# Kernel tuning notes

Hardware: AMD Instinct MI355X
Metric: run time of the kernel (lower is better)

The kernel has to match this reference:

```python
import jax, jax.numpy as jnp
import numpy as np

S, B, E = 2048, 8, 1024  # seq_len, batch, embed_dim
GAMMA = 0.5              # Kernel(gamma=0.5)


def setup_inputs() -> dict:
    key = jax.random.key(0)
    ks = jax.random.split(key, 4)
    # Weight scale 1/E keeps pairwise squared distances O(1) so the RBF
    # kernel weights are well-conditioned (exp doesn't underflow to all-zeros).
    w_scale = 1.0 / E
    inputs = jax.random.normal(ks[0], (S, B, E), dtype=jnp.float32)
    Wq = jax.random.normal(ks[1], (E, E), dtype=jnp.float32) * w_scale
    Wk = jax.random.normal(ks[2], (E, E), dtype=jnp.float32) * w_scale
    Wv = jax.random.normal(ks[3], (E, E), dtype=jnp.float32) * w_scale
    bq = jnp.zeros((E,), jnp.float32)
    bk = jnp.zeros((E,), jnp.float32)
    bv = jnp.zeros((E,), jnp.float32)
    return {"inputs": inputs, "Wq": Wq, "bq": bq, "Wk": Wk, "bk": bk,
            "Wv": Wv, "bv": bv}


def reference(inputs, Wq, bq, Wk, bk, Wv, bv):
    # QKV projections (nn.Linear: x @ W.T + b)
    q = inputs @ Wq.T + bq  # (S, B, E)
    k = inputs @ Wk.T + bk  # (S, B, E)
    v = inputs @ Wv.T + bv  # (S, B, E)

    # Pairwise RBF kernel sim[t, j, b] = exp(-gamma * ||q[t,b] - k[j,b]||^2)
    # (vectorized replacement of the original O(S^2) python double loop),
    # via ||q||^2 + ||k||^2 - 2 q.k expansion (GEMM-shaped contraction).
    q2 = jnp.sum(q * q, axis=-1)                 # (S, B)
    k2 = jnp.sum(k * k, axis=-1)                 # (S, B)
    qk = jnp.einsum('tbe,jbe->tjb', q, k)        # (S, S, B)
    d2 = q2[:, None, :] + k2[None, :, :] - 2.0 * qk
    d2 = jnp.maximum(d2, 0.0)

    # sim / sim.sum(dim=1) with sim = exp(-gamma*d2) is exactly
    # softmax(-gamma*d2) over axis 1 (the j axis) -- numerically stable form.
    sim = jax.nn.softmax(-GAMMA * d2, axis=1)    # (S, S, B): (t, j, b)

    # Aggregate values: out[t, b, e] = sum_j sim[t, j, b] * v[j, b, e]
    return jnp.einsum('tjb,jbe->tbe', sim, v)    # (S, B, E)
```

## Files before the change

### kernel.cpp

```cpp
#include <hip/hip_runtime.h>
#include <stdint.h>

#define S_LEN 2048
#define BATCH 8
#define EMB   1024
#define GAMMA 0.5f

typedef unsigned short ushort_t;
typedef __attribute__((ext_vector_type(8))) short  short8;
typedef __attribute__((ext_vector_type(8))) unsigned short ushort8;
typedef __attribute__((ext_vector_type(4))) float  floatx4;

__device__ __forceinline__ ushort_t f2bf(float f) {
  uint32_t x = __float_as_uint(f);
  x += 0x7fffu + ((x >> 16) & 1u);
  return (ushort_t)(x >> 16);
}

__device__ __forceinline__ void gl_lds16(const ushort_t* g, ushort_t* l) {
  __builtin_amdgcn_global_load_lds(
      (const __attribute__((address_space(1))) unsigned int*)g,
      (__attribute__((address_space(3))) unsigned int*)l, 16, 0, 0);
}


__device__ __forceinline__ void stage_half(const ushort_t* __restrict__ G,
                                           int ld, int kcol,
                                           ushort_t* lregion, int wave, int lane) {
  const int r4 = lane >> 2;
  const int slot = (lane & 3) ^ ((r4 >> 1) & 3);
  const ushort_t* g = G + (size_t)(wave * 32 + r4) * ld + kcol + slot * 8;
  gl_lds16(g, lregion + wave * 1024);
  gl_lds16(g + (size_t)16 * ld, lregion + wave * 1024 + 512);
}

__device__ __forceinline__ short8 lds_frag(const ushort_t* region, int row, int q) {
  return *(const short8*)(region + row * 32 + (((q ^ (row >> 1)) & 3) << 3));
}

#define MFMA_PH(J0, J1)                                                        \
  __builtin_amdgcn_s_barrier();                                                \
  asm volatile("s_waitcnt lgkmcnt(0)" ::: "memory");                           \
  __builtin_amdgcn_sched_barrier(0);                                           \
  __builtin_amdgcn_s_setprio(1);                                               \
  _Pragma("unroll")                                                            \
  for (int i = 0; i < 8; ++i) {                                                \
    acc[i][J0] = __builtin_amdgcn_mfma_f32_16x16x32_bf16(ar[i], b0, acc[i][J0], 0, 0, 0); \
    acc[i][J1] = __builtin_amdgcn_mfma_f32_16x16x32_bf16(ar[i], b1, acc[i][J1], 0, 0, 0); \
  }                                                                            \
  __builtin_amdgcn_s_setprio(0);

__device__ __forceinline__ void gemm8_core(
    const ushort_t* __restrict__ A, const ushort_t* __restrict__ B,
    int lda, int ldb, int K, ushort_t* smem, floatx4 (&acc)[8][4])
{
  const int tid = threadIdx.x;
  const int wave = tid >> 6, lane = tid & 63;
  const int wm = wave >> 2, wn = wave & 3;
  const int lr = lane & 15, q = lane >> 4;
  const int NT = K >> 6;

  stage_half(A, lda, 0,  smem +     0, wave, lane);
  stage_half(B, ldb, 0,  smem + 16384, wave, lane);
  stage_half(A, lda, 32, smem +  8192, wave, lane);
  stage_half(B, ldb, 32, smem + 24576, wave, lane);
  stage_half(A, lda, 64, smem + 32768, wave, lane);
  stage_half(B, ldb, 64, smem + 49152, wave, lane);
  stage_half(A, lda, 96, smem + 40960, wave, lane);
  asm volatile("s_waitcnt vmcnt(6)" ::: "memory");
  __builtin_amdgcn_s_barrier();
  __builtin_amdgcn_sched_barrier(0);

  const int ra = wm * 128 + lr;
  const int rb = wn * 64 + lr;
  short8 ar[8], b0, b1;

  for (int kt = 0; kt < NT; ++kt) {
    ushort_t* const cur = smem + (kt & 1) * 32768;
    ushort_t* const nxt = smem + ((kt & 1) ^ 1) * 32768;
    const bool st2 = (kt + 2) < NT;

#pragma unroll
    for (int i = 0; i < 8; ++i) ar[i] = lds_frag(cur, ra + i * 16, q);
    b0 = lds_frag(cur + 16384, rb,      q);
    b1 = lds_frag(cur + 16384, rb + 16, q);
    if (kt + 1 < NT) stage_half(B, ldb, (kt + 1) * 64 + 32, nxt + 24576, wave, lane);
    MFMA_PH(0, 1)
    __builtin_amdgcn_s_barrier();

    b0 = lds_frag(cur + 16384, rb + 32, q);
    b1 = lds_frag(cur + 16384, rb + 48, q);
    if (st2) stage_half(A, lda, (kt + 2) * 64, cur, wave, lane);
    MFMA_PH(2, 3)
    __builtin_amdgcn_s_barrier();

#pragma unroll
    for (int i = 0; i < 8; ++i) ar[i] = lds_frag(cur + 8192, ra + i * 16, q);
    b0 = lds_frag(cur + 24576, rb,      q);
    b1 = lds_frag(cur + 24576, rb + 16, q);
    if (st2) stage_half(B, ldb, (kt + 2) * 64, cur + 16384, wave, lane);
    MFMA_PH(0, 1)
    __builtin_amdgcn_s_barrier();

    b0 = lds_frag(cur + 24576, rb + 32, q);
    b1 = lds_frag(cur + 24576, rb + 48, q);
    if (st2) stage_half(A, lda, (kt + 2) * 64 + 32, cur + 8192, wave, lane);
    MFMA_PH(2, 3)
    if (st2)              { asm volatile("s_waitcnt vmcnt(6)" ::: "memory"); }
    else if (kt + 1 < NT) { asm volatile("s_waitcnt vmcnt(0)" ::: "memory"); }
    __builtin_amdgcn_s_barrier();
  }
}

__global__ __launch_bounds__(256) void k_quant_x(const float* __restrict__ X,
                                                 ushort_t* __restrict__ Xb) {
  size_t i = ((size_t)blockIdx.x * 256 + threadIdx.x) * 4;
  float4 v = *(const float4*)(X + i);
  *(ushort4*)(Xb + i) = make_ushort4(f2bf(v.x), f2bf(v.y), f2bf(v.z), f2bf(v.w));
}

__global__ __launch_bounds__(256) void k_quant_w(
    const float* __restrict__ Wq, const float* __restrict__ Wk,
    const float* __restrict__ Wv, ushort_t* __restrict__ W) {
  size_t i = ((size_t)blockIdx.x * 256 + threadIdx.x) * 4;
  int row = (int)(i >> 10), col = (int)(i & 1023);
  int sel = row >> 10, sr = row & 1023;
  const float* src = sel == 0 ? Wq : (sel == 1 ? Wk : Wv);
  float4 v = *(const float4*)(src + (size_t)sr * 1024 + col);
  *(ushort4*)(W + i) = make_ushort4(f2bf(v.x), f2bf(v.y), f2bf(v.z), f2bf(v.w));
}

__global__ __launch_bounds__(256) void k_bias_zero(
    const float* __restrict__ bq, const float* __restrict__ bk,
    const float* __restrict__ bv, float* __restrict__ bias,
    float* __restrict__ q2, float* __restrict__ k2, float* __restrict__ rsum) {
  int i = blockIdx.x * 256 + threadIdx.x;
  if (i < 1024)       bias[i] = bq[i];
  else if (i < 2048)  bias[i] = bk[i - 1024];
  else if (i < 3072)  bias[i] = bv[i - 2048];
  if (i < BATCH * S_LEN) { q2[i] = 0.f; k2[i] = 0.f; rsum[i] = 0.f; }
}

__global__ __launch_bounds__(512, 2) void k_gemm_qkv(
    const ushort_t* __restrict__ Xb, const ushort_t* __restrict__ W,
    const float* __restrict__ bias,
    ushort_t* __restrict__ Q, ushort_t* __restrict__ Kp, ushort_t* __restrict__ V,
    float* __restrict__ q2, float* __restrict__ k2) {
  __shared__ __attribute__((aligned(16))) ushort_t smem[65536];
  const int mt = blockIdx.x * 256, nt = blockIdx.y * 256;
  floatx4 acc[8][4];
  const floatx4 z = {0.f, 0.f, 0.f, 0.f};
#pragma unroll
  for (int i = 0; i < 8; ++i)
#pragma unroll
    for (int j = 0; j < 4; ++j) acc[i][j] = z;

  gemm8_core(Xb + (size_t)mt * EMB, W + (size_t)nt * EMB, EMB, EMB, EMB, smem, acc);

  const int lane = threadIdx.x & 63, wave = threadIdx.x >> 6;
  const int wm = wave >> 2, wn = wave & 3;
  const int lr = lane & 15, q = lane >> 4;
  const int which = nt >> 10;
  const int nc0 = nt & 1023;
  ushort_t* dst = which == 0 ? Q : (which == 1 ? Kp : V);
  float* sq = which == 0 ? q2 : k2;
  float bv4[4];
#pragma unroll
  for (int j = 0; j < 4; ++j) bv4[j] = bias[nt + wn * 64 + j * 16 + lr];

#pragma unroll
  for (int i = 0; i < 8; ++i) {
#pragma unroll
    for (int r = 0; r < 4; ++r) {
      const int g = mt + wm * 128 + i * 16 + q * 4 + r;
      const int t = g >> 3, b = g & 7;
      float ss = 0.f;
#pragma unroll
      for (int j = 0; j < 4; ++j) {
        const float val = acc[i][j][r] + bv4[j];
        dst[(size_t)(b * S_LEN + t) * EMB + nc0 + wn * 64 + j * 16 + lr] = f2bf(val);
        ss += val * val;
      }
      if (which < 2) {
        ss += __shfl_xor(ss, 1);
        ss += __shfl_xor(ss, 2);
        ss += __shfl_xor(ss, 4);
        ss += __shfl_xor(ss, 8);
        if (lr == 0) atomicAdd(&sq[b * S_LEN + t], ss);
      }
    }
  }
}

__global__ __launch_bounds__(256) void k_transpose(const ushort_t* __restrict__ V,
                                                   ushort_t* __restrict__ Vt) {
  __shared__ ushort_t tile[64][72];
  const int b = blockIdx.z, j0 = blockIdx.x * 64, e0 = blockIdx.y * 64;
  const ushort_t* src = V + ((size_t)b * S_LEN + j0) * EMB + e0;
  const int tid = threadIdx.x;
#pragma unroll
  for (int rep = 0; rep < 2; ++rep) {
    const int lin = rep * 256 + tid;
    const int j = lin >> 3, e8 = (lin & 7) * 8;
    *(uint4*)&tile[j][e8] = *(const uint4*)(src + (size_t)j * EMB + e8);
  }
  __syncthreads();
  ushort_t* dst = Vt + ((size_t)b * EMB + e0) * S_LEN + j0;
#pragma unroll
  for (int rep = 0; rep < 2; ++rep) {
    const int lin = rep * 256 + tid;
    const int e = lin >> 3, j8 = (lin & 7) * 8;
    ushort8 o;
#pragma unroll
    for (int m = 0; m < 8; ++m) o[m] = tile[j8 + m][e];
    *(ushort8*)(dst + (size_t)e * S_LEN + j8) = o;
  }
}

__global__ __launch_bounds__(512, 2) void k_logits(
    const ushort_t* __restrict__ Q, const ushort_t* __restrict__ Kp,
    const float* __restrict__ q2, const float* __restrict__ k2,
    ushort_t* __restrict__ P, float* __restrict__ rsum) {
  __shared__ __attribute__((aligned(16))) ushort_t smem[65536];
  const int b = blockIdx.z;
  const int mt = blockIdx.x * 256, nt = blockIdx.y * 256;
  floatx4 acc[8][4];
  const floatx4 z = {0.f, 0.f, 0.f, 0.f};
#pragma unroll
  for (int i = 0; i < 8; ++i)
#pragma unroll
    for (int j = 0; j < 4; ++j) acc[i][j] = z;

  gemm8_core(Q + ((size_t)b * S_LEN + mt) * EMB,
             Kp + ((size_t)b * S_LEN + nt) * EMB, EMB, EMB, EMB, smem, acc);

  const int lane = threadIdx.x & 63, wave = threadIdx.x >> 6;
  const int wm = wave >> 2, wn = wave & 3;
  const int lr = lane & 15, q = lane >> 4;
  float k2v[4];
#pragma unroll
  for (int j = 0; j < 4; ++j) k2v[j] = k2[b * S_LEN + nt + wn * 64 + j * 16 + lr];

#pragma unroll
  for (int i = 0; i < 8; ++i) {
#pragma unroll
    for (int r = 0; r < 4; ++r) {
      const int t = mt + wm * 128 + i * 16 + q * 4 + r;
      const float q2v = q2[b * S_LEN + t];
      float ss = 0.f;
#pragma unroll
      for (int j = 0; j < 4; ++j) {
        float d2 = q2v + k2v[j] - 2.f * acc[i][j][r];
        d2 = fmaxf(d2, 0.f);
        const float p = __expf(-GAMMA * d2);
        P[((size_t)b * S_LEN + t) * S_LEN + nt + wn * 64 + j * 16 + lr] = f2bf(p);
        ss += p;
      }
      ss += __shfl_xor(ss, 1);
      ss += __shfl_xor(ss, 2);
      ss += __shfl_xor(ss, 4);
      ss += __shfl_xor(ss, 8);
      if (lr == 0) atomicAdd(&rsum[b * S_LEN + t], ss);
    }
  }
}

__global__ __launch_bounds__(512, 2) void k_out(
    const ushort_t* __restrict__ P, const ushort_t* __restrict__ Vt,
    const float* __restrict__ rsum, float* __restrict__ out) {
  __shared__ __attribute__((aligned(16))) ushort_t smem[65536];
  const int b = blockIdx.z;
  const int mt = blockIdx.x * 256, nt = blockIdx.y * 256;
  floatx4 acc[8][4];
  const floatx4 z = {0.f, 0.f, 0.f, 0.f};
#pragma unroll
  for (int i = 0; i < 8; ++i)
#pragma unroll
    for (int j = 0; j < 4; ++j) acc[i][j] = z;

  gemm8_core(P + ((size_t)b * S_LEN + mt) * S_LEN,
             Vt + ((size_t)b * EMB + nt) * S_LEN, S_LEN, S_LEN, S_LEN, smem, acc);

  const int lane = threadIdx.x & 63, wave = threadIdx.x >> 6;
  const int wm = wave >> 2, wn = wave & 3;
  const int lr = lane & 15, q = lane >> 4;
#pragma unroll
  for (int i = 0; i < 8; ++i) {
#pragma unroll
    for (int r = 0; r < 4; ++r) {
      const int t = mt + wm * 128 + i * 16 + q * 4 + r;
      const float rinv = 1.f / rsum[b * S_LEN + t];
#pragma unroll
      for (int j = 0; j < 4; ++j) {
        const int e = nt + wn * 64 + j * 16 + lr;
        out[((size_t)t * BATCH + b) * EMB + e] = acc[i][j][r] * rinv;
      }
    }
  }
}

extern "C" void kernel_launch(void* const* d_in, const int* in_sizes, int n_in,
                              void* d_out, int out_size, void* d_ws, size_t ws_size,
                              hipStream_t stream) {
  (void)in_sizes; (void)n_in; (void)out_size; (void)ws_size;
  const float* X  = (const float*)d_in[0];
  const float* Wq = (const float*)d_in[1];
  const float* bq = (const float*)d_in[2];
  const float* Wk = (const float*)d_in[3];
  const float* bk = (const float*)d_in[4];
  const float* Wv = (const float*)d_in[5];
  const float* bv = (const float*)d_in[6];
  float* out = (float*)d_out;
  char* ws = (char*)d_ws;

  ushort_t* Q    = (ushort_t*)(ws + 0);
  ushort_t* Kp   = (ushort_t*)(ws + 33554432);
  ushort_t* V    = (ushort_t*)(ws + 67108864);
  ushort_t* Vt   = (ushort_t*)(ws + 100663296);
  ushort_t* P    = (ushort_t*)(ws + 134217728);
  ushort_t* Xb   = (ushort_t*)(ws + 134217728);
  ushort_t* Wqkv = (ushort_t*)(ws + 201326592);
  float*    bias = (float*)(ws + 207618048);
  float*    q2   = (float*)(ws + 207630336);
  float*    k2   = (float*)(ws + 207695872);
  float*    rsum = (float*)(ws + 207761408);

  k_quant_x <<<16384, 256, 0, stream>>>(X, Xb);
  k_quant_w <<<3072, 256, 0, stream>>>(Wq, Wk, Wv, Wqkv);
  k_bias_zero<<<64, 256, 0, stream>>>(bq, bk, bv, bias, q2, k2, rsum);
  k_gemm_qkv<<<dim3(64, 12), 512, 0, stream>>>(Xb, Wqkv, bias, Q, Kp, V, q2, k2);
  k_transpose<<<dim3(32, 16, 8), 256, 0, stream>>>(V, Vt);
  k_logits  <<<dim3(8, 8, 8), 512, 0, stream>>>(Q, Kp, q2, k2, P, rsum);
  k_out     <<<dim3(8, 4, 8), 512, 0, stream>>>(P, Vt, rsum, out);
}
```

Before: 407.9 us.

## Software-pipeline LDS fragment loads one MFMA phase ahead in GEMM core

Restructures the GEMM main loop so that the LDS fragment reads for the next MFMA phase are issued right after the current phase's MFMAs, double-buffering the register fragments (ar/ar2, t/u). The aim is to hide LDS read latency behind matrix-core work instead of waiting on lgkmcnt right before each MFMA burst. Barriers are reduced to one per interval, and the vmcnt waits are retuned. This costs extra VGPRs for the second fragment set and makes the barrier/wait ordering around buffer reuse more delicate.

After: 403.4 us. Within noise of the previous version (-1.1%).

```diff
diff --git a/kernel.cpp b/kernel.cpp
--- a/kernel.cpp
+++ b/kernel.cpp
@@ -38,17 +38,19 @@
   return *(const short8*)(region + row * 32 + (((q ^ (row >> 1)) & 3) << 3));
 }
 
-#define MFMA_PH(J0, J1)                                                        \
-  __builtin_amdgcn_s_barrier();                                                \
-  asm volatile("s_waitcnt lgkmcnt(0)" ::: "memory");                           \
-  __builtin_amdgcn_sched_barrier(0);                                           \
+#define MFMA_16(AR, B0, B1, J0, J1)                                            \
   __builtin_amdgcn_s_setprio(1);                                               \
   _Pragma("unroll")                                                            \
   for (int i = 0; i < 8; ++i) {                                                \
-    acc[i][J0] = __builtin_amdgcn_mfma_f32_16x16x32_bf16(ar[i], b0, acc[i][J0], 0, 0, 0); \
-    acc[i][J1] = __builtin_amdgcn_mfma_f32_16x16x32_bf16(ar[i], b1, acc[i][J1], 0, 0, 0); \
+    acc[i][J0] = __builtin_amdgcn_mfma_f32_16x16x32_bf16(AR[i], B0, acc[i][J0], 0, 0, 0); \
+    acc[i][J1] = __builtin_amdgcn_mfma_f32_16x16x32_bf16(AR[i], B1, acc[i][J1], 0, 0, 0); \
   }                                                                            \
   __builtin_amdgcn_s_setprio(0);
+
+#define INTERVAL_OPEN()                                                        \
+  __builtin_amdgcn_s_barrier();                                                \
+  asm volatile("s_waitcnt lgkmcnt(0)" ::: "memory");                           \
+  __builtin_amdgcn_sched_barrier(0);
 
 __device__ __forceinline__ void gemm8_core(
     const ushort_t* __restrict__ A, const ushort_t* __restrict__ B,
@@ -59,6 +61,8 @@
   const int wm = wave >> 2, wn = wave & 3;
   const int lr = lane & 15, q = lane >> 4;
   const int NT = K >> 6;
+  const int ra = wm * 128 + lr;
+  const int rb = wn * 64 + lr;
 
   stage_half(A, lda, 0,  smem +     0, wave, lane);
   stage_half(B, ldb, 0,  smem + 16384, wave, lane);
@@ -71,44 +75,52 @@
   __builtin_amdgcn_s_barrier();
   __builtin_amdgcn_sched_barrier(0);
 
-  const int ra = wm * 128 + lr;
-  const int rb = wn * 64 + lr;
-  short8 ar[8], b0, b1;
+  short8 ar[8], ar2[8], b0, b1, t0, t1, u0, u1;
+#pragma unroll
+  for (int i = 0; i < 8; ++i) ar[i] = lds_frag(smem, ra + i * 16, q);
+  b0 = lds_frag(smem + 16384, rb,      q);
+  b1 = lds_frag(smem + 16384, rb + 16, q);
 
   for (int kt = 0; kt < NT; ++kt) {
     ushort_t* const cur = smem + (kt & 1) * 32768;
     ushort_t* const nxt = smem + ((kt & 1) ^ 1) * 32768;
-    const bool st2 = (kt + 2) < NT;
-
-#pragma unroll
-    for (int i = 0; i < 8; ++i) ar[i] = lds_frag(cur, ra + i * 16, q);
-    b0 = lds_frag(cur + 16384, rb,      q);
-    b1 = lds_frag(cur + 16384, rb + 16, q);
-    if (kt + 1 < NT) stage_half(B, ldb, (kt + 1) * 64 + 32, nxt + 24576, wave, lane);
-    MFMA_PH(0, 1)
-    __builtin_amdgcn_s_barrier();
-
-    b0 = lds_frag(cur + 16384, rb + 32, q);
-    b1 = lds_frag(cur + 16384, rb + 48, q);
-    if (st2) stage_half(A, lda, (kt + 2) * 64, cur, wave, lane);
-    MFMA_PH(2, 3)
-    __builtin_amdgcn_s_barrier();
-
-#pragma unroll
-    for (int i = 0; i < 8; ++i) ar[i] = lds_frag(cur + 8192, ra + i * 16, q);
-    b0 = lds_frag(cur + 24576, rb,      q);
-    b1 = lds_frag(cur + 24576, rb + 16, q);
-    if (st2) stage_half(B, ldb, (kt + 2) * 64, cur + 16384, wave, lane);
-    MFMA_PH(0, 1)
-    __builtin_amdgcn_s_barrier();
-
-    b0 = lds_frag(cur + 24576, rb + 32, q);
-    b1 = lds_frag(cur + 24576, rb + 48, q);
-    if (st2) stage_half(A, lda, (kt + 2) * 64 + 32, cur + 8192, wave, lane);
-    MFMA_PH(2, 3)
-    if (st2)              { asm volatile("s_waitcnt vmcnt(6)" ::: "memory"); }
-    else if (kt + 1 < NT) { asm volatile("s_waitcnt vmcnt(0)" ::: "memory"); }
-    __builtin_amdgcn_s_barrier();
+    const bool s1 = (kt + 1) < NT, s2 = (kt + 2) < NT;
+
+    INTERVAL_OPEN()
+    MFMA_16(ar, b0, b1, 0, 1)
+    t0 = lds_frag(cur + 16384, rb + 32, q);
+    t1 = lds_frag(cur + 16384, rb + 48, q);
+#pragma unroll
+    for (int i = 0; i < 4; ++i) ar2[i] = lds_frag(cur + 8192, ra + i * 16, q);
+    if (s1) stage_half(B, ldb, (kt + 1) * 64 + 32, nxt + 24576, wave, lane);
+
+    INTERVAL_OPEN()
+    MFMA_16(ar, t0, t1, 2, 3)
+#pragma unroll
+    for (int i = 4; i < 8; ++i) ar2[i] = lds_frag(cur + 8192, ra + i * 16, q);
+    u0 = lds_frag(cur + 24576, rb,      q);
+    u1 = lds_frag(cur + 24576, rb + 16, q);
+    if (s2) stage_half(A, lda, (kt + 2) * 64, cur, wave, lane);
+
+    INTERVAL_OPEN()
+    MFMA_16(ar2, u0, u1, 0, 1)
+    t0 = lds_frag(cur + 24576, rb + 32, q);
+    t1 = lds_frag(cur + 24576, rb + 48, q);
+    if (s2) stage_half(B, ldb, (kt + 2) * 64, cur + 16384, wave, lane);
+    if (s1) {
+      if (s2) { asm volatile("s_waitcnt vmcnt(4)" ::: "memory"); }
+      else    { asm volatile("s_waitcnt vmcnt(0)" ::: "memory"); }
+    }
+
+    INTERVAL_OPEN()
+    MFMA_16(ar2, t0, t1, 2, 3)
+    if (s1) {
+#pragma unroll
+      for (int i = 0; i < 8; ++i) ar[i] = lds_frag(nxt, ra + i * 16, q);
+      b0 = lds_frag(nxt + 16384, rb,      q);
+      b1 = lds_frag(nxt + 16384, rb + 16, q);
+    }
+    if (s2) stage_half(A, lda, (kt + 2) * 64 + 32, cur + 8192, wave, lane);
   }
 }
 
```
